# Performance work log

Hardware: AMD Instinct MI355X
Metric: run time of the kernel (lower is better)

Reference implementation:

```python
import jax, jax.numpy as jnp
import numpy as np

N_HEAD = 16
HEAD_DIM = 32          # n_embed // n_head // 2
LAMBDA_INIT = 0.2      # 0.8 - 0.6*exp(-0.3*(layer-1)) with layer=1
ROPE_BASE = 10000.0
EPS = 1e-5


def _rope(x):
    # torchtune RotaryPositionalEmbeddings: interleaved adjacent pairs
    B, T, H, D = x.shape
    half = D // 2
    theta = ROPE_BASE ** (-(jnp.arange(half, dtype=jnp.float32) * 2.0 / D))  # [half]
    ang = jnp.arange(T, dtype=jnp.float32)[:, None] * theta[None, :]         # [T, half]
    cos = jnp.cos(ang)[None, :, None, :]
    sin = jnp.sin(ang)[None, :, None, :]
    xr = x.reshape(B, T, H, half, 2)
    x1, x2 = xr[..., 0], xr[..., 1]
    out = jnp.stack([x1 * cos - x2 * sin, x1 * sin + x2 * cos], axis=-1)
    return out.reshape(B, T, H, D).astype(x.dtype)


def reference(x, W_attn, W_proj, lambda_q1, lambda_k1, lambda_q2, lambda_k2):
    B, T, C = x.shape
    H, D = N_HEAD, HEAD_DIM
    qkv = x @ W_attn                              # [B,T,3C]
    q, k, v = jnp.split(qkv, 3, axis=-1)
    q = _rope(q.reshape(B, T, 2 * H, D)).transpose(0, 2, 1, 3)   # [B,2H,T,D]
    k = _rope(k.reshape(B, T, 2 * H, D)).transpose(0, 2, 1, 3)   # [B,2H,T,D]
    v = v.reshape(B, T, H, 2 * D).transpose(0, 2, 1, 3)          # [B,H,T,2D]

    lam = (jnp.exp(jnp.dot(lambda_q1, lambda_k1))
           - jnp.exp(jnp.dot(lambda_q2, lambda_k2)) + LAMBDA_INIT)

    # causal SDPA over both score paths (2H heads) in one pass, shared V
    scale = 1.0 / jnp.sqrt(jnp.asarray(D, x.dtype))
    scores = jnp.einsum('bhqd,bhkd->bhqk', q, k) * scale         # [B,2H,T,T]
    causal = jnp.tril(jnp.ones((T, T), dtype=bool))
    scores = jnp.where(causal, scores, jnp.finfo(scores.dtype).min)
    probs = jax.nn.softmax(scores, axis=-1)
    vv = jnp.concatenate([v, v], axis=1)                         # [B,2H,T,2D]
    A = jnp.einsum('bhqk,bhkd->bhqd', probs, vv)                 # [B,2H,T,2D]
    A1, A2 = A[:, :H], A[:, H:]

    diff = A1 - lam * A2                                         # [B,H,T,2D]
    # RMSNorm over last dim (2*head_dim), no affine, eps=1e-5
    diff = diff * jax.lax.rsqrt(jnp.mean(diff * diff, axis=-1, keepdims=True) + EPS)
    diff = (1.0 - LAMBDA_INIT) * diff
    out = diff.transpose(0, 2, 1, 3).reshape(B, T, C)
    return out @ W_proj


def setup_inputs() -> dict:
    key = jax.random.key(0)
    ks = jax.random.split(key, 7)
    B, T, C, D = 2, 2048, 1024, HEAD_DIM
    return {
        'x': jax.random.normal(ks[0], (B, T, C), jnp.float32),
        'W_attn': jax.random.normal(ks[1], (C, 3 * C), jnp.float32) * 0.02,
        'W_proj': jax.random.normal(ks[2], (C, C), jnp.float32) * 0.02,
        'lambda_q1': jax.random.normal(ks[3], (D,), jnp.float32) * 0.1,
        'lambda_k1': jax.random.normal(ks[4], (D,), jnp.float32) * 0.1,
        'lambda_q2': jax.random.normal(ks[5], (D,), jnp.float32) * 0.1,
        'lambda_k2': jax.random.normal(ks[6], (D,), jnp.float32) * 0.1,
    }
```

## Files before the change

### kernel.cpp

```cpp
#include <hip/hip_runtime.h>


typedef unsigned short u16;
typedef __bf16 bf16x8 __attribute__((ext_vector_type(8)));
typedef float f32x4 __attribute__((ext_vector_type(4)));
typedef float f32x16 __attribute__((ext_vector_type(16)));
typedef unsigned u32x2 __attribute__((ext_vector_type(2)));

__device__ __forceinline__ u16 f2bf(float f) {
  return __builtin_bit_cast(u16, (__bf16)f);
}
__device__ __forceinline__ float bf2f(u16 u) {
  return (float)__builtin_bit_cast(__bf16, u);
}
__device__ __forceinline__ unsigned pk2(float a, float b) {
  return (unsigned)f2bf(a) | ((unsigned)f2bf(b) << 16);
}

__device__ __forceinline__ void gload16(const u16* g, u16* l) {
  __builtin_amdgcn_global_load_lds(
      (const __attribute__((address_space(1))) unsigned int*)g,
      (__attribute__((address_space(3))) unsigned int*)l, 16, 0, 0);
}

__device__ __forceinline__ void trans_body(const float* __restrict__ in,
                                           u16* __restrict__ out, int R, int Cn,
                                           int bx, int by, float (*tile)[33],
                                           int tx, int ty) {
  const int c0 = bx * 32, r0 = by * 32;
#pragma unroll
  for (int rr = 0; rr < 4; ++rr)
    tile[ty + rr * 8][tx] = in[(size_t)(r0 + ty + rr * 8) * Cn + c0 + tx];
  __syncthreads();
#pragma unroll
  for (int rr = 0; rr < 4; ++rr)
    out[(size_t)(c0 + ty + rr * 8) * R + r0 + tx] = f2bf(tile[tx][ty + rr * 8]);
}

__global__ __launch_bounds__(256) void prep_kernel(
    const float* __restrict__ x, const float* __restrict__ Wa,
    const float* __restrict__ Wp, const float* __restrict__ lq1,
    const float* __restrict__ lk1, const float* __restrict__ lq2,
    const float* __restrict__ lk2, u16* __restrict__ xb, u16* __restrict__ WaT,
    u16* __restrict__ WpT, float2* __restrict__ Tab, float* __restrict__ lamp) {
  __shared__ float tile[32][33];
  const int id = blockIdx.x;
  const int tx = threadIdx.x & 31, ty = threadIdx.x >> 5;
  if (id < 4096) {
    const int i = id * 256 + threadIdx.x;
    float4 v = ((const float4*)x)[i];
    ushort4 o;
    o.x = f2bf(v.x); o.y = f2bf(v.y); o.z = f2bf(v.z); o.w = f2bf(v.w);
    ((ushort4*)xb)[i] = o;
  } else if (id < 7168) {
    const int t = id - 4096;
    trans_body(Wa, WaT, 1024, 3072, t % 96, t / 96, tile, tx, ty);
  } else if (id < 8192) {
    const int t = id - 7168;
    trans_body(Wp, WpT, 1024, 1024, t & 31, t >> 5, tile, tx, ty);
  } else if (id < 8320) {
    const int idx = (id - 8192) * 256 + threadIdx.x;
    const int t = idx >> 4, i = idx & 15;
    const float theta = exp2f(-0.83048202372184059f * (float)i);
    float sn, cs;
    sincosf((float)t * theta, &sn, &cs);
    Tab[idx] = make_float2(cs, sn);
  } else if (threadIdx.x == 0) {
    float d1 = 0.f, d2 = 0.f;
#pragma unroll
    for (int i = 0; i < 32; ++i) {
      d1 += lq1[i] * lk1[i];
      d2 += lq2[i] * lk2[i];
    }
    *lamp = expf(d1) - expf(d2) + 0.2f;
  }
}

__global__ __launch_bounds__(256, 3) void gemm_qkv_kernel(
    const u16* __restrict__ A, const u16* __restrict__ BT,
    u16* __restrict__ Q, u16* __restrict__ K, u16* __restrict__ VT,
    const float2* __restrict__ Tab) {
  const int Kdim = 1024;
  __shared__ u16 SH[24576];
  const int tid = threadIdx.x;
  const int l = tid & 63;
  const int w = tid >> 6;
  const int nwgx = gridDim.x;
  const int lin = blockIdx.x + nwgx * blockIdx.y;
  const int cpx = (nwgx * gridDim.y) >> 3;
  const int swz = (lin & 7) * cpx + (lin >> 3);
  const int bm = swz / nwgx, bn = swz % nwgx;
  const int wm = w >> 1, wn = w & 1;
  const int rowA0 = bm * 64, rowB0 = bn * 128;
  const int r_ = tid >> 2;
  const int s_ = (tid & 3) * 8;
  const u16* Ag = &A[(size_t)(rowA0 + r_) * Kdim + s_];
  const u16* Bg = &BT[(size_t)(rowB0 + r_) * Kdim + s_];
  const size_t rstride = (size_t)64 * Kdim;
  f32x4 acc[2][4] = {};
  const int nt = 32;
#pragma unroll
  for (int p = 0; p < 3; ++p) {
    u16* D = SH + p * 6144;
    const int k1 = p * 32;
    gload16(Ag + k1, &D[tid * 8]);
    gload16(Bg + k1, &D[2048 + tid * 8]);
    gload16(Bg + rstride + k1, &D[4096 + tid * 8]);
  }
  asm volatile("s_waitcnt vmcnt(6)" ::: "memory");
  __builtin_amdgcn_s_barrier();
  __builtin_amdgcn_sched_barrier(0);
  for (int t = 0; t < nt; ++t) {
    if (t + 3 < nt) {
      u16* D = SH + ((t + 3) & 3) * 6144;
      const int k1 = (t + 3) * 32;
      gload16(Ag + k1, &D[tid * 8]);
      gload16(Bg + k1, &D[2048 + tid * 8]);
      gload16(Bg + rstride + k1, &D[4096 + tid * 8]);
    }
    const u16* Asc = SH + (t & 3) * 6144;
    const u16* Bsc = Asc + 2048;
    bf16x8 a[2], b[4];
#pragma unroll
    for (int i = 0; i < 2; ++i)
      a[i] = *(const bf16x8*)&Asc[(wm * 32 + i * 16 + (l & 15)) * 32 + (l >> 4) * 8];
#pragma unroll
    for (int j = 0; j < 4; ++j)
      b[j] = *(const bf16x8*)&Bsc[(wn * 64 + j * 16 + (l & 15)) * 32 + (l >> 4) * 8];
    __builtin_amdgcn_s_setprio(1);
#pragma unroll
    for (int i = 0; i < 2; ++i)
#pragma unroll
      for (int j = 0; j < 4; ++j)
        acc[i][j] = __builtin_amdgcn_mfma_f32_16x16x32_bf16(a[i], b[j], acc[i][j], 0, 0, 0);
    __builtin_amdgcn_s_setprio(0);
    if (t + 1 < nt) {
      if (t + 3 < nt)
        asm volatile("s_waitcnt vmcnt(6)" ::: "memory");
      else if (t + 2 < nt)
        asm volatile("s_waitcnt vmcnt(3)" ::: "memory");
      else
        asm volatile("s_waitcnt vmcnt(0)" ::: "memory");
      __builtin_amdgcn_s_barrier();
      __builtin_amdgcn_sched_barrier(0);
    }
  }
  const int cr = (l >> 4) * 4;
  const int cc = l & 15;
  const int region = bn >> 3;
  const int b_ = rowA0 >> 11, tb = rowA0 & 2047;
  if (region < 2) {
    const float qsc_ = (region == 0) ? 0.25503486f : 1.0f;
    u16* dst = (region == 0) ? Q : K;
#pragma unroll
    for (int i = 0; i < 2; ++i) {
      const int trow0 = wm * 32 + i * 16 + cr;
#pragma unroll
      for (int j = 0; j < 4; ++j) {
        const int c = (bn & 7) * 128 + wn * 64 + j * 16 + cc;
        const int hh = c >> 5, d = c & 31;
        const int ii = d >> 1;
        const float sgn = (d & 1) ? 1.0f : -1.0f;
        const size_t base = (size_t)(b_ * 32 + hh) * 2048;
#pragma unroll
        for (int r = 0; r < 4; ++r) {
          const int t = tb + trow0 + r;
          const float2 cs = Tab[t * 16 + ii];
          const float xv = acc[i][j][r];
          const float px = __shfl_xor(xv, 1, 64);
          dst[(base + t) * 32 + d] = f2bf((xv * cs.x + sgn * px * cs.y) * qsc_);
        }
      }
    }
  } else {
#pragma unroll
    for (int i = 0; i < 2; ++i) {
      const int t0 = tb + wm * 32 + i * 16 + cr;
#pragma unroll
      for (int j = 0; j < 4; ++j) {
        const int c3 = (bn & 7) * 128 + wn * 64 + j * 16 + cc;
        const int hv = c3 >> 6, dv = c3 & 63;
        ushort4 ov;
        ov.x = f2bf(acc[i][j][0]);
        ov.y = f2bf(acc[i][j][1]);
        ov.z = f2bf(acc[i][j][2]);
        ov.w = f2bf(acc[i][j][3]);
        *(ushort4*)&VT[((size_t)(b_ * 16 + hv) * 64 + dv) * 2048 + t0] = ov;
      }
    }
  }
}

__global__ __launch_bounds__(256, 3) void gemm_out_kernel(
    const u16* __restrict__ A, const u16* __restrict__ BT, float* __restrict__ Cout,
    int Mdim, int Ndim, int Kdim) {
  __shared__ u16 SH[24576];
  const int tid = threadIdx.x;
  const int l = tid & 63;
  const int w = tid >> 6;
  const int nwgx = gridDim.x;
  const int lin = blockIdx.x + nwgx * blockIdx.y;
  const int cpx = (nwgx * gridDim.y) >> 3;
  const int swz = (lin & 7) * cpx + (lin >> 3);
  const int bm = swz / nwgx, bn = swz % nwgx;
  const int wm = w >> 1, wn = w & 1;
  const int rowA0 = bm * 64, rowB0 = bn * 128;
  const int r_ = tid >> 2;
  const int s_ = (tid & 3) * 8;
  const u16* Ag = &A[(size_t)(rowA0 + r_) * Kdim + s_];
  const u16* Bg = &BT[(size_t)(rowB0 + r_) * Kdim + s_];
  const size_t rstride = (size_t)64 * Kdim;
  f32x4 acc[2][4] = {};
  const int nt = Kdim >> 5;
#pragma unroll
  for (int p = 0; p < 3; ++p) {
    u16* D = SH + p * 6144;
    const int k1 = p * 32;
    gload16(Ag + k1, &D[tid * 8]);
    gload16(Bg + k1, &D[2048 + tid * 8]);
    gload16(Bg + rstride + k1, &D[4096 + tid * 8]);
  }
  asm volatile("s_waitcnt vmcnt(6)" ::: "memory");
  __builtin_amdgcn_s_barrier();
  __builtin_amdgcn_sched_barrier(0);
  for (int t = 0; t < nt; ++t) {
    if (t + 3 < nt) {
      u16* D = SH + ((t + 3) & 3) * 6144;
      const int k1 = (t + 3) * 32;
      gload16(Ag + k1, &D[tid * 8]);
      gload16(Bg + k1, &D[2048 + tid * 8]);
      gload16(Bg + rstride + k1, &D[4096 + tid * 8]);
    }
    const u16* Asc = SH + (t & 3) * 6144;
    const u16* Bsc = Asc + 2048;
    bf16x8 a[2], b[4];
#pragma unroll
    for (int i = 0; i < 2; ++i)
      a[i] = *(const bf16x8*)&Asc[(wm * 32 + i * 16 + (l & 15)) * 32 + (l >> 4) * 8];
#pragma unroll
    for (int j = 0; j < 4; ++j)
      b[j] = *(const bf16x8*)&Bsc[(wn * 64 + j * 16 + (l & 15)) * 32 + (l >> 4) * 8];
    __builtin_amdgcn_s_setprio(1);
#pragma unroll
    for (int i = 0; i < 2; ++i)
#pragma unroll
      for (int j = 0; j < 4; ++j)
        acc[i][j] = __builtin_amdgcn_mfma_f32_16x16x32_bf16(a[i], b[j], acc[i][j], 0, 0, 0);
    __builtin_amdgcn_s_setprio(0);
    if (t + 1 < nt) {
      if (t + 3 < nt)
        asm volatile("s_waitcnt vmcnt(6)" ::: "memory");
      else if (t + 2 < nt)
        asm volatile("s_waitcnt vmcnt(3)" ::: "memory");
      else
        asm volatile("s_waitcnt vmcnt(0)" ::: "memory");
      __builtin_amdgcn_s_barrier();
      __builtin_amdgcn_sched_barrier(0);
    }
  }
  const int cr = (l >> 4) * 4;
  const int cc = l & 15;
#pragma unroll
  for (int i = 0; i < 2; ++i)
#pragma unroll
    for (int j = 0; j < 4; ++j)
#pragma unroll
      for (int r = 0; r < 4; ++r) {
        const int row = rowA0 + wm * 32 + i * 16 + cr + r;
        const int col = rowB0 + wn * 64 + j * 16 + cc;
        Cout[(size_t)row * Ndim + col] = acc[i][j][r];
      }
}

__global__ __launch_bounds__(256, 4) void attn_kernel(const u16* __restrict__ Q,
                                                      const u16* __restrict__ K,
                                                      const u16* __restrict__ VT,
                                                      u16* __restrict__ PO0,
                                                      u16* __restrict__ PO1,
                                                      float* __restrict__ ML) {
  __shared__ u16 Ks[64 * 34];
  __shared__ u16 Vs[64 * 66];
  __shared__ u16 Os[4 * 32 * 66];
  const int tid = threadIdx.x, l = tid & 63, w = tid >> 6;
  const int pp = blockIdx.x & 7, hf = blockIdx.x >> 3;
  const int h = blockIdx.y, b = blockIdx.z;
  const size_t qkbase = (size_t)(b * 32 + h) * 2048;
  const size_t vtb = (size_t)(b * 16 + (h & 15)) * 64;
  const int lq = l & 31, hi = l >> 5;
  const f32x16 z16 = {};
  const int krow = tid >> 2, ksl = (tid & 3) * 8;
  const int dva = tid >> 3, vsl = (tid & 7) * 8;
  const int dvb = dva + 32;
  const __bf16 one1 = (__bf16)1.0f;
  const bf16x8 ones = {one1, one1, one1, one1, one1, one1, one1, one1};

  for (int halfidx = 0; halfidx < 2; ++halfidx) {
    const int qt = halfidx ? (15 - pp) : pp;
    const int slot = hf ^ halfidx;
    const int s_begin = slot ? (qt + 1) : 0;
    const int s_end = slot ? (2 * qt + 2) : (qt + 1);
    const int q0 = qt * 128;
    const int qw = q0 + w * 32;
    const int q = qw + lq;
    const bf16x8 qf0 = *(const bf16x8*)&Q[(qkbase + q) * 32 + hi * 8];
    const bf16x8 qf1 = *(const bf16x8*)&Q[(qkbase + q) * 32 + 16 + hi * 8];
    f32x16 olo = {}, ohi = {}, lacc = {};
    uint4 kreg = *(const uint4*)&K[(qkbase + s_begin * 64 + krow) * 32 + ksl];
    uint4 vreg0 = *(const uint4*)&VT[(vtb + dva) * 2048 + s_begin * 64 + vsl];
    uint4 vreg1 = *(const uint4*)&VT[(vtb + dvb) * 2048 + s_begin * 64 + vsl];
    for (int s = s_begin; s < s_end; ++s) {
      const int kb = s * 64;
      *(uint4*)&Ks[krow * 34 + ksl] = kreg;
      *(uint4*)&Vs[dva * 66 + vsl] = vreg0;
      *(uint4*)&Vs[dvb * 66 + vsl] = vreg1;
      const int sn = (s + 1 < s_end) ? (s + 1) : s;
      kreg = *(const uint4*)&K[(qkbase + sn * 64 + krow) * 32 + ksl];
      vreg0 = *(const uint4*)&VT[(vtb + dva) * 2048 + sn * 64 + vsl];
      vreg1 = *(const uint4*)&VT[(vtb + dvb) * 2048 + sn * 64 + vsl];
      __syncthreads();
      if (qw + 31 >= kb) {
        f32x16 s0_, s1_;
        {
          const bf16x8 ka0 = *(const bf16x8*)&Ks[lq * 34 + hi * 8];
          const bf16x8 ka1 = *(const bf16x8*)&Ks[lq * 34 + 16 + hi * 8];
          const bf16x8 kc0 = *(const bf16x8*)&Ks[(32 + lq) * 34 + hi * 8];
          const bf16x8 kc1 = *(const bf16x8*)&Ks[(32 + lq) * 34 + 16 + hi * 8];
          __builtin_amdgcn_s_setprio(1);
          s0_ = __builtin_amdgcn_mfma_f32_32x32x16_bf16(ka0, qf0, z16, 0, 0, 0);
          s0_ = __builtin_amdgcn_mfma_f32_32x32x16_bf16(ka1, qf1, s0_, 0, 0, 0);
          s1_ = __builtin_amdgcn_mfma_f32_32x32x16_bf16(kc0, qf0, z16, 0, 0, 0);
          s1_ = __builtin_amdgcn_mfma_f32_32x32x16_bf16(kc1, qf1, s1_, 0, 0, 0);
          __builtin_amdgcn_s_setprio(0);
        }
        const bool nm = (kb + 63 > qw);
        if (nm) {
#pragma unroll
          for (int r = 0; r < 16; ++r) {
            const int kr = (r & 3) + 8 * (r >> 2) + 4 * hi;
            if (kb + kr > q) s0_[r] = -1e30f;
            if (kb + 32 + kr > q) s1_[r] = -1e30f;
          }
        }
#pragma unroll
        for (int r = 0; r < 16; ++r) {
          s0_[r] = __builtin_amdgcn_exp2f(s0_[r]);
          s1_[r] = __builtin_amdgcn_exp2f(s1_[r]);
        }
        unsigned pw[16];
#pragma unroll
        for (int j = 0; j < 8; ++j) {
          pw[j] = pk2(s0_[2 * j], s0_[2 * j + 1]);
          pw[8 + j] = pk2(s1_[2 * j], s1_[2 * j + 1]);
        }
        bf16x8 pa[4];
#pragma unroll
        for (int fidx = 0; fidx < 4; ++fidx) {
          const unsigned* wt = &pw[fidx * 4];
          union { unsigned u[4]; bf16x8 v; } fr;
#if __has_builtin(__builtin_amdgcn_permlane32_swap)
          const u32x2 rA = __builtin_amdgcn_permlane32_swap(wt[0], wt[2], false, false);
          const u32x2 rB = __builtin_amdgcn_permlane32_swap(wt[1], wt[3], false, false);
          fr.u[0] = rA[0]; fr.u[1] = rB[0]; fr.u[2] = rA[1]; fr.u[3] = rB[1];
#else
          const unsigned ua = hi ? wt[0] : wt[2];
          const unsigned ub = hi ? wt[1] : wt[3];
          const unsigned sa = __shfl_xor(ua, 32, 64);
          const unsigned sb = __shfl_xor(ub, 32, 64);
          fr.u[0] = hi ? sa : wt[0];
          fr.u[1] = hi ? sb : wt[1];
          fr.u[2] = hi ? wt[2] : sa;
          fr.u[3] = hi ? wt[3] : sb;
#endif
          pa[fidx] = fr.v;
        }
        __builtin_amdgcn_s_setprio(1);
#pragma unroll
        for (int ks = 0; ks < 4; ++ks) {
          const bf16x8 va = *(const bf16x8*)&Vs[lq * 66 + ks * 16 + hi * 8];
          const bf16x8 vb = *(const bf16x8*)&Vs[(32 + lq) * 66 + ks * 16 + hi * 8];
          olo = __builtin_amdgcn_mfma_f32_32x32x16_bf16(va, pa[ks], olo, 0, 0, 0);
          ohi = __builtin_amdgcn_mfma_f32_32x32x16_bf16(vb, pa[ks], ohi, 0, 0, 0);
          lacc = __builtin_amdgcn_mfma_f32_32x32x16_bf16(ones, pa[ks], lacc, 0, 0, 0);
        }
        __builtin_amdgcn_s_setprio(0);
      }
      __syncthreads();
    }
    const float lsum = lacc[0];
    const float inv = (lsum > 0.f) ? (1.0f / lsum) : 0.f;
    if (hi == 0)
      ML[(size_t)slot * 131072 + qkbase + q] = lsum;
    u16* Ow = &Os[(w * 32 + lq) * 66];
#pragma unroll
    for (int g = 0; g < 4; ++g) {
      const int d0 = 8 * g + 4 * hi;
      *(unsigned*)&Ow[d0] = pk2(olo[4 * g] * inv, olo[4 * g + 1] * inv);
      *(unsigned*)&Ow[d0 + 2] = pk2(olo[4 * g + 2] * inv, olo[4 * g + 3] * inv);
      *(unsigned*)&Ow[32 + d0] = pk2(ohi[4 * g] * inv, ohi[4 * g + 1] * inv);
      *(unsigned*)&Ow[32 + d0 + 2] = pk2(ohi[4 * g + 2] * inv, ohi[4 * g + 3] * inv);
    }
    __syncthreads();
    u16* PO = slot ? PO1 : PO0;
    for (int s2 = tid; s2 < 1024; s2 += 256) {
      const int wv = s2 >> 8, qq = (s2 >> 3) & 31, sl = (s2 & 7) * 8;
      *(uint4*)&PO[(qkbase + q0 + wv * 32 + qq) * 64 + sl] =
          *(const uint4*)&Os[(wv * 32 + qq) * 66 + sl];
    }
    __syncthreads();
  }
}

__global__ __launch_bounds__(256) void diff_rms_kernel(
    const u16* __restrict__ PO0, const u16* __restrict__ PO1,
    const float* __restrict__ ML, const float* __restrict__ lamp,
    u16* __restrict__ Mb) {
  const int g = threadIdx.x >> 5;
  const int dl = (threadIdx.x & 31) * 2;
  const int ridx = blockIdx.x * 8 + g;
  const int b = ridx >> 15, rem = ridx & 32767, h = rem >> 11, t = rem & 2047;
  const float lam = *lamp;
  const size_t row1 = (size_t)(b * 32 + h) * 2048 + t;
  const size_t row2 = (size_t)(b * 32 + 16 + h) * 2048 + t;
  const float lA1 = ML[row1], lB1 = ML[131072 + row1];
  const float lA2 = ML[row2], lB2 = ML[131072 + row2];
  const float i1 = 1.0f / (lA1 + lB1);
  const float wa1 = lA1 * i1, wb1 = lB1 * i1;
  const float i2 = 1.0f / (lA2 + lB2);
  const float wa2 = lA2 * i2, wb2 = lB2 * i2;
  const ushort2 p01 = *(const ushort2*)&PO0[row1 * 64 + dl];
  const ushort2 p11 = *(const ushort2*)&PO1[row1 * 64 + dl];
  const ushort2 p02 = *(const ushort2*)&PO0[row2 * 64 + dl];
  const ushort2 p12 = *(const ushort2*)&PO1[row2 * 64 + dl];
  const float a1x = wa1 * bf2f(p01.x) + wb1 * bf2f(p11.x);
  const float a1y = wa1 * bf2f(p01.y) + wb1 * bf2f(p11.y);
  const float a2x = wa2 * bf2f(p02.x) + wb2 * bf2f(p12.x);
  const float a2y = wa2 * bf2f(p02.y) + wb2 * bf2f(p12.y);
  const float df0 = a1x - lam * a2x;
  const float df1 = a1y - lam * a2y;
  float ss = df0 * df0 + df1 * df1;
  ss += __shfl_xor(ss, 1, 64);
  ss += __shfl_xor(ss, 2, 64);
  ss += __shfl_xor(ss, 4, 64);
  ss += __shfl_xor(ss, 8, 64);
  ss += __shfl_xor(ss, 16, 64);
  const float rms = rsqrtf(ss * (1.0f / 64.0f) + 1e-5f);
  ushort2 o;
  o.x = f2bf(0.8f * df0 * rms);
  o.y = f2bf(0.8f * df1 * rms);
  *(ushort2*)&Mb[((size_t)(b * 2048 + t)) * 1024 + h * 64 + dl] = o;
}

extern "C" void kernel_launch(void* const* d_in, const int* in_sizes, int n_in,
                              void* d_out, int out_size, void* d_ws, size_t ws_size,
                              hipStream_t stream) {
  const float* x = (const float*)d_in[0];
  const float* Wa = (const float*)d_in[1];
  const float* Wp = (const float*)d_in[2];
  const float* lq1 = (const float*)d_in[3];
  const float* lk1 = (const float*)d_in[4];
  const float* lq2 = (const float*)d_in[5];
  const float* lk2 = (const float*)d_in[6];
  if (ws_size < (size_t)(64u << 20)) return;

  char* ws = (char*)d_ws;
  u16* Qarr = (u16*)(ws);
  u16* Karr = (u16*)(ws + (8u << 20));
  u16* VTarr = (u16*)(ws + (16u << 20));
  u16* WpT = (u16*)(ws + (24u << 20));
  char* arena = ws + (26u << 20);
  u16* xb = (u16*)(arena);
  u16* WaT = (u16*)(arena + (8u << 20));
  float2* Tab = (float2*)(arena + (14u << 20));
  u16* PO0 = (u16*)(arena);
  u16* PO1 = (u16*)(arena + (16u << 20));
  float* ML = (float*)(arena + (32u << 20));
  float* lamp = (float*)(arena + (33u << 20));
  u16* Mbuf = Qarr;

  prep_kernel<<<8321, 256, 0, stream>>>(x, Wa, Wp, lq1, lk1, lq2, lk2,
                                        xb, WaT, WpT, Tab, lamp);
  gemm_qkv_kernel<<<dim3(24, 64), 256, 0, stream>>>(xb, WaT, Qarr, Karr, VTarr, Tab);
  attn_kernel<<<dim3(16, 32, 2), 256, 0, stream>>>(Qarr, Karr, VTarr, PO0, PO1, ML);
  diff_rms_kernel<<<8192, 256, 0, stream>>>(PO0, PO1, ML, lamp, Mbuf);
  gemm_out_kernel<<<dim3(8, 64), 256, 0, stream>>>(Mbuf, WpT, (float*)d_out, 4096, 1024, 1024);
}
```

Before: 138.9 us.

## Enlarge QKV GEMM tile to 256x128 with 512 threads and double buffering

The QKV projection GEMM moves from 64x128 tiles with 4 waves to 256x128 tiles with 8 waves, each wave now holding a 64x64 accumulator. This cuts the grid to a quarter as many workgroups and should reduce redundant loads of the weight matrix. The hand-tuned 4-stage LDS pipeline with explicit vmcnt waits is replaced by a simple 2-stage double buffer synchronised with __syncthreads, so there is less load-latency hiding. The larger accumulator under the new launch bounds may also push register pressure high enough to cause spills.

```diff
diff --git a/kernel.cpp b/kernel.cpp
--- a/kernel.cpp
+++ b/kernel.cpp
@@ -76,7 +76,7 @@
   }
 }
 
-__global__ __launch_bounds__(256, 3) void gemm_qkv_kernel(
+__global__ __launch_bounds__(512, 4) void gemm_qkv_kernel(
     const u16* __restrict__ A, const u16* __restrict__ BT,
     u16* __restrict__ Q, u16* __restrict__ K, u16* __restrict__ VT,
     const float2* __restrict__ Tab) {
@@ -91,59 +91,44 @@
   const int swz = (lin & 7) * cpx + (lin >> 3);
   const int bm = swz / nwgx, bn = swz % nwgx;
   const int wm = w >> 1, wn = w & 1;
-  const int rowA0 = bm * 64, rowB0 = bn * 128;
+  const int rowA0 = bm * 256, rowB0 = bn * 128;
   const int r_ = tid >> 2;
   const int s_ = (tid & 3) * 8;
-  const u16* Ag = &A[(size_t)(rowA0 + r_) * Kdim + s_];
+  const u16* Ag0 = &A[(size_t)(rowA0 + r_) * Kdim + s_];
+  const u16* Ag1 = Ag0 + (size_t)128 * Kdim;
   const u16* Bg = &BT[(size_t)(rowB0 + r_) * Kdim + s_];
-  const size_t rstride = (size_t)64 * Kdim;
-  f32x4 acc[2][4] = {};
-  const int nt = 32;
-#pragma unroll
-  for (int p = 0; p < 3; ++p) {
-    u16* D = SH + p * 6144;
-    const int k1 = p * 32;
-    gload16(Ag + k1, &D[tid * 8]);
-    gload16(Bg + k1, &D[2048 + tid * 8]);
-    gload16(Bg + rstride + k1, &D[4096 + tid * 8]);
-  }
-  asm volatile("s_waitcnt vmcnt(6)" ::: "memory");
-  __builtin_amdgcn_s_barrier();
-  __builtin_amdgcn_sched_barrier(0);
-  for (int t = 0; t < nt; ++t) {
-    if (t + 3 < nt) {
-      u16* D = SH + ((t + 3) & 3) * 6144;
-      const int k1 = (t + 3) * 32;
-      gload16(Ag + k1, &D[tid * 8]);
-      gload16(Bg + k1, &D[2048 + tid * 8]);
-      gload16(Bg + rstride + k1, &D[4096 + tid * 8]);
-    }
-    const u16* Asc = SH + (t & 3) * 6144;
-    const u16* Bsc = Asc + 2048;
-    bf16x8 a[2], b[4];
-#pragma unroll
-    for (int i = 0; i < 2; ++i)
-      a[i] = *(const bf16x8*)&Asc[(wm * 32 + i * 16 + (l & 15)) * 32 + (l >> 4) * 8];
+  f32x4 acc[4][4] = {};
+  gload16(Ag0, &SH[tid * 8]);
+  gload16(Ag1, &SH[4096 + tid * 8]);
+  gload16(Bg, &SH[8192 + tid * 8]);
+  __syncthreads();
+  int cur = 0;
+  for (int t = 0; t < 32; ++t) {
+    const u16* Asc = SH + cur * 12288;
+    const u16* Bsc = Asc + 8192;
+    if (t + 1 < 32) {
+      u16* D = SH + (cur ^ 1) * 12288;
+      const int k1 = (t + 1) * 32;
+      gload16(Ag0 + k1, &D[tid * 8]);
+      gload16(Ag1 + k1, &D[4096 + tid * 8]);
+      gload16(Bg + k1, &D[8192 + tid * 8]);
+    }
+    bf16x8 a[4], b[4];
+#pragma unroll
+    for (int i = 0; i < 4; ++i)
+      a[i] = *(const bf16x8*)&Asc[(wm * 64 + i * 16 + (l & 15)) * 32 + (l >> 4) * 8];
 #pragma unroll
     for (int j = 0; j < 4; ++j)
       b[j] = *(const bf16x8*)&Bsc[(wn * 64 + j * 16 + (l & 15)) * 32 + (l >> 4) * 8];
     __builtin_amdgcn_s_setprio(1);
 #pragma unroll
-    for (int i = 0; i < 2; ++i)
+    for (int i = 0; i < 4; ++i)
 #pragma unroll
       for (int j = 0; j < 4; ++j)
         acc[i][j] = __builtin_amdgcn_mfma_f32_16x16x32_bf16(a[i], b[j], acc[i][j], 0, 0, 0);
     __builtin_amdgcn_s_setprio(0);
-    if (t + 1 < nt) {
-      if (t + 3 < nt)
-        asm volatile("s_waitcnt vmcnt(6)" ::: "memory");
-      else if (t + 2 < nt)
-        asm volatile("s_waitcnt vmcnt(3)" ::: "memory");
-      else
-        asm volatile("s_waitcnt vmcnt(0)" ::: "memory");
-      __builtin_amdgcn_s_barrier();
-      __builtin_amdgcn_sched_barrier(0);
-    }
+    __syncthreads();
+    cur ^= 1;
   }
   const int cr = (l >> 4) * 4;
   const int cc = l & 15;
@@ -153,8 +138,8 @@
     const float qsc_ = (region == 0) ? 0.25503486f : 1.0f;
     u16* dst = (region == 0) ? Q : K;
 #pragma unroll
-    for (int i = 0; i < 2; ++i) {
-      const int trow0 = wm * 32 + i * 16 + cr;
+    for (int i = 0; i < 4; ++i) {
+      const int trow0 = wm * 64 + i * 16 + cr;
 #pragma unroll
       for (int j = 0; j < 4; ++j) {
         const int c = (bn & 7) * 128 + wn * 64 + j * 16 + cc;
@@ -174,8 +159,8 @@
     }
   } else {
 #pragma unroll
-    for (int i = 0; i < 2; ++i) {
-      const int t0 = tb + wm * 32 + i * 16 + cr;
+    for (int i = 0; i < 4; ++i) {
+      const int t0 = tb + wm * 64 + i * 16 + cr;
 #pragma unroll
       for (int j = 0; j < 4; ++j) {
         const int c3 = (bn & 7) * 128 + wn * 64 + j * 16 + cc;
@@ -479,7 +464,7 @@
 
   prep_kernel<<<8321, 256, 0, stream>>>(x, Wa, Wp, lq1, lk1, lq2, lk2,
                                         xb, WaT, WpT, Tab, lamp);
-  gemm_qkv_kernel<<<dim3(24, 64), 256, 0, stream>>>(xb, WaT, Qarr, Karr, VTarr, Tab);
+  gemm_qkv_kernel<<<dim3(24, 16), 512, 0, stream>>>(xb, WaT, Qarr, Karr, VTarr, Tab);
   attn_kernel<<<dim3(16, 32, 2), 256, 0, stream>>>(Qarr, Karr, VTarr, PO0, PO1, ML);
   diff_rms_kernel<<<8192, 256, 0, stream>>>(PO0, PO1, ML, lamp, Mbuf);
   gemm_out_kernel<<<dim3(8, 64), 256, 0, stream>>>(Mbuf, WpT, (float*)d_out, 4096, 1024, 1024);
```

Measured after the change: 124.1 us, median of 3. -10.7%, faster.
